# Performance work log

Measured on AMD Instinct MI355X. Metric: run time of the kernel, lower is better.

## Reference

```python
import jax, jax.numpy as jnp
import numpy as np

B, N, DIN = 16, 1024, 256
HEADS, OUT_DIM = 4, 256
F = OUT_DIM // HEADS  # per-head feature dim
NEG_SLOPE = 0.2
MASK_VAL = -1e9


def setup_inputs() -> dict:
    key = jax.random.key(0)
    k1, k2, k3, k4, k5, k6 = jax.random.split(key, 6)
    x = jax.random.normal(k1, (B, N, DIN), dtype=jnp.float32)
    adj = jax.random.uniform(k2, (B, N, N), dtype=jnp.float32)  # >0.5 -> edge
    # GATConv learned params (Glorot-ish scale)
    W = jax.random.normal(k3, (DIN, HEADS, F), dtype=jnp.float32) * (1.0 / np.sqrt(DIN))
    a_src = jax.random.normal(k4, (HEADS, F), dtype=jnp.float32) * (1.0 / np.sqrt(F))
    a_dst = jax.random.normal(k5, (HEADS, F), dtype=jnp.float32) * (1.0 / np.sqrt(F))
    bias = jax.random.normal(k6, (OUT_DIM,), dtype=jnp.float32) * 0.01
    return {"x": x, "adj": adj, "W": W, "a_src": a_src, "a_dst": a_dst, "bias": bias}


def reference(x, adj, W, a_src, a_dst, bias):
    # GAT over a dense adjacency mask: mathematically identical to
    # per-sample tf.where edge extraction + edge-list GATConv (softmax over
    # j with adj[b,i,j] > 0.5), but fully vectorized over the batch.
    b, n, _ = x.shape
    h = jnp.einsum('bnd,dhf->bnhf', x, W)                  # [B,N,H,F]
    e_src = jnp.einsum('bnhf,hf->bhn', h, a_src)           # source logits
    e_dst = jnp.einsum('bnhf,hf->bhn', h, a_dst)           # target logits
    # e[b,h,i,j]: edge j -> i
    e = e_dst[:, :, :, None] + e_src[:, :, None, :]        # [B,H,N,N]
    e = jax.nn.leaky_relu(e, NEG_SLOPE)
    mask = (adj > 0.5)[:, None, :, :]                      # [B,1,N,N]
    e = jnp.where(mask, e, MASK_VAL)
    attn = jax.nn.softmax(e, axis=-1)                      # softmax over sources j
    out = jnp.einsum('bhij,bjhf->bihf', attn, h)           # aggregate messages
    out = out.reshape(b, n, HEADS * F) + bias              # concat heads + bias
    return out
```

## Files before the change

### kernel.cpp

```cpp
#include <hip/hip_runtime.h>

#define B_    16
#define N_    1024
#define DIN_  256
#define H_    4
#define F_    64
#define COUT_ 256
#define NEG_  0.2f
#define LOG2E_ 1.4426950408889634f

typedef __bf16 bf16x8 __attribute__((ext_vector_type(8)));
typedef float  f32x4  __attribute__((ext_vector_type(4)));
typedef unsigned short u16x8 __attribute__((ext_vector_type(8)));
typedef unsigned short u16x4 __attribute__((ext_vector_type(4)));
typedef unsigned int   u32x4 __attribute__((ext_vector_type(4)));

__device__ __forceinline__ unsigned short f2bf(float f) {
    unsigned u = __builtin_bit_cast(unsigned, f);
    u += 0x7fffu + ((u >> 16) & 1u);
    return (unsigned short)(u >> 16);
}

__global__ __launch_bounds__(256) void prep_kernel(
    const float* __restrict__ W, unsigned short* __restrict__ Wtp) {
    const int c = blockIdx.x, k = threadIdx.x;
    const int w = c >> 6, ft = (c >> 4) & 3, l15 = c & 15;
    const int it = k >> 5, q = (k >> 3) & 3, jj = k & 7;
    const int ln = q * 16 + l15;
    Wtp[((((w * 8 + it) * 4 + ft) * 64) + ln) * 8 + jj] = f2bf(W[k * COUT_ + c]);
}

__global__ __launch_bounds__(256, 4) void stage_kernel(
    const float* __restrict__ adj, const float* __restrict__ x,
    const unsigned short* __restrict__ Wtp, const float* __restrict__ a_src,
    const float* __restrict__ a_dst, unsigned int* __restrict__ mask,
    unsigned short* __restrict__ hp, float* __restrict__ e_src,
    float* __restrict__ e_dst) {
    __shared__ unsigned short xs[16][264];
    const int w  = threadIdx.x >> 6;
    const int ln = threadIdx.x & 63;

    if (blockIdx.x < 4096) {
        const int row = blockIdx.x * 4 + w;
        const int b = row >> 10, i = row & (N_ - 1);
        const float* ar = adj + (size_t)row * N_ + ln * 4;
#pragma unroll
        for (int c = 0; c < 4; c++) {
            f32x4 v = *(const f32x4*)(ar + c * 256);
            unsigned nib = 0;
#pragma unroll
            for (int e = 0; e < 4; e++)
                nib |= (v[e] > 0.5f) ? (1u << e) : 0u;
            unsigned word = nib << ((ln & 7) * 4);
            word |= __shfl_xor(word, 1);
            word |= __shfl_xor(word, 2);
            word |= __shfl_xor(word, 4);
            if ((ln & 7) == 0) {
                const int jc = c * 8 + (ln >> 3);
                mask[(b * 32 + jc) * N_ + i] = word;
            }
        }
    } else {
        const int blk = blockIdx.x - 4096;
        const int b   = blk & 15;
        const int it0 = (blk >> 4) * 16;
        const int l15 = ln & 15;
        const int q   = ln >> 4;

#pragma unroll
        for (int s = 0; s < 4; s++) {
            const int row = w * 4 + s;
            f32x4 xv = *(const f32x4*)(x + (size_t)(b * N_ + it0 + row) * DIN_ + ln * 4);
            unsigned lo = (unsigned)f2bf(xv[0]) | ((unsigned)f2bf(xv[1]) << 16);
            unsigned hi = (unsigned)f2bf(xv[2]) | ((unsigned)f2bf(xv[3]) << 16);
            unsigned long long hb = (unsigned long long)lo | ((unsigned long long)hi << 32);
            *(unsigned long long*)&xs[row][ln * 4] = hb;
        }
        __syncthreads();

        f32x4 acc[4];
#pragma unroll
        for (int ft = 0; ft < 4; ft++) acc[ft] = (f32x4)0.0f;

        const unsigned short* wb = Wtp + (w * 8) * 4 * 64 * 8 + ln * 8;
#pragma unroll
        for (int it = 0; it < 8; it++) {
            bf16x8 af = *(const bf16x8*)&xs[l15][it * 32 + q * 8];
#pragma unroll
            for (int ft = 0; ft < 4; ft++) {
                bf16x8 bf = *((const bf16x8*)(wb + (it * 4 + ft) * 512));
                acc[ft] = __builtin_amdgcn_mfma_f32_16x16x32_bf16(af, bf, acc[ft], 0, 0, 0);
            }
        }

        const int jg = it0 >> 5;
        const int q2 = 2 * ((it0 >> 4) & 1) + (q >> 1);
#pragma unroll
        for (int ft = 0; ft < 4; ft++) {
            u16x4 hb;
#pragma unroll
            for (int r = 0; r < 4; r++) hb[r] = f2bf(acc[ft][r]);
            const size_t addr =
                (size_t)((((b * H_ + w) * 32 + jg) * 4 + ft) * 64 + q2 * 16 + l15) * 8 + (q & 1) * 4;
            *((u16x4*)(hp + addr)) = hb;
        }

        float as_v[4], ad_v[4];
#pragma unroll
        for (int ft = 0; ft < 4; ft++) {
            as_v[ft] = a_src[w * F_ + ft * 16 + l15];
            ad_v[ft] = a_dst[w * F_ + ft * 16 + l15];
        }
        float ps[4], pd[4];
#pragma unroll
        for (int r = 0; r < 4; r++) {
            ps[r] = 0.0f; pd[r] = 0.0f;
#pragma unroll
            for (int ft = 0; ft < 4; ft++) {
                ps[r] += acc[ft][r] * as_v[ft];
                pd[r] += acc[ft][r] * ad_v[ft];
            }
        }
#pragma unroll
        for (int off = 1; off <= 8; off <<= 1)
#pragma unroll
            for (int r = 0; r < 4; r++) {
                ps[r] += __shfl_xor(ps[r], off);
                pd[r] += __shfl_xor(pd[r], off);
            }
        float vs = (l15 == 0) ? ps[0] : (l15 == 1) ? ps[1] : (l15 == 2) ? ps[2] : ps[3];
        float vd = (l15 == 0) ? pd[0] : (l15 == 1) ? pd[1] : (l15 == 2) ? pd[2] : pd[3];
        if (l15 < 4) {
            const int i = it0 + q * 4 + l15;
            e_src[(b * H_ + w) * N_ + i] = vs * LOG2E_;
            e_dst[(b * H_ + w) * N_ + i] = vd * LOG2E_;
        }
    }
}

__global__ __launch_bounds__(512, 4) void gat_attn_kernel(
    const unsigned int* __restrict__ mask, const unsigned short* __restrict__ hp,
    const float* __restrict__ e_src, const float* __restrict__ e_dst,
    const float* __restrict__ bias, float* __restrict__ out) {
    const int lid = ((blockIdx.x & 7) << 6) | (blockIdx.x >> 3);
    const int b   = lid >> 5;
    const int it0 = (lid & 31) * 32;
    const int w8  = threadIdx.x >> 6;
    const int h   = w8 & 3;
    const int jh  = w8 >> 2;
    const int ln  = threadIdx.x & 63;
    const int l15 = ln & 15;
    const int q   = ln >> 4;

    __shared__ float lds[H_][2][5][64][4];
    __shared__ float es_s[H_][N_];
    __shared__ unsigned mk_s[32][32];

    {
        const int tid = threadIdx.x;
#pragma unroll
        for (int p = 0; p < 2; p++) {
            const int c  = p * 512 + tid;
            const int h_ = c >> 8;
            const int of = (c & 255) * 4;
            *(f32x4*)&es_s[h_][of] =
                *(const f32x4*)(e_src + (size_t)(b * H_ + h_) * N_ + of);
        }
        if (tid < 256) {
            const int jc = tid >> 3;
            const int i4 = (tid & 7) * 4;
            *(u32x4*)&mk_s[jc][i4] =
                *(const u32x4*)(mask + (size_t)(b * 32 + jc) * N_ + it0 + i4);
        }
    }

    float edv[2];
    edv[0] = e_dst[(b * H_ + h) * N_ + it0 + l15];
    edv[1] = e_dst[(b * H_ + h) * N_ + it0 + 16 + l15];

    const unsigned short* hp_base = hp + (size_t)((b * H_ + h) * 32) * 2048 + ln * 8;

    f32x4 acc[2][4];
    f32x4 accs[2];
#pragma unroll
    for (int mt = 0; mt < 2; mt++) {
#pragma unroll
        for (int ft = 0; ft < 4; ft++) acc[mt][ft] = (f32x4)0.0f;
        accs[mt] = (f32x4)0.0f;
    }

    u16x8 ones_u;
#pragma unroll
    for (int jj = 0; jj < 8; jj++) ones_u[jj] = 0x3F80;
    const bf16x8 ones = __builtin_bit_cast(bf16x8, ones_u);

    __syncthreads();

    const unsigned short* hf0 = hp_base + (size_t)(jh * 16) * 2048;
    bf16x8 nb0 = *((const bf16x8*)(hf0 + 0 * 512));
    bf16x8 nb1 = *((const bf16x8*)(hf0 + 1 * 512));
    bf16x8 nb2 = *((const bf16x8*)(hf0 + 2 * 512));
    bf16x8 nb3 = *((const bf16x8*)(hf0 + 3 * 512));

#pragma unroll
    for (int t = 0; t < 16; t++) {
        const int jg = jh * 16 + t;
        const bf16x8 cb0 = nb0, cb1 = nb1, cb2 = nb2, cb3 = nb3;
        if (t < 15) {
            const unsigned short* hfn = hp_base + (size_t)(jg + 1) * 2048;
            nb0 = *((const bf16x8*)(hfn + 0 * 512));
            nb1 = *((const bf16x8*)(hfn + 1 * 512));
            nb2 = *((const bf16x8*)(hfn + 2 * 512));
            nb3 = *((const bf16x8*)(hfn + 3 * 512));
        }

        f32x4 e0 = *(const f32x4*)&es_s[h][jg * 32 + q * 8];
        f32x4 e1 = *(const f32x4*)&es_s[h][jg * 32 + q * 8 + 4];
        const unsigned m0 = mk_s[jg][l15];
        const unsigned m1 = mk_s[jg][16 + l15];

        float es8[8] = {e0[0], e0[1], e0[2], e0[3], e1[0], e1[1], e1[2], e1[3]};

        bf16x8 afr[2];
#pragma unroll
        for (int mt = 0; mt < 2; mt++) {
            const unsigned mq = ((mt ? m1 : m0) >> (q * 8)) & 0xffu;
            u32x4 up;
#pragma unroll
            for (int p2 = 0; p2 < 4; p2++) {
                float t0 = edv[mt] + es8[2 * p2];
                float t1 = edv[mt] + es8[2 * p2 + 1];
                t0 = fmaxf(t0, NEG_ * t0);
                t1 = fmaxf(t1, NEG_ * t1);
                float p0 = __builtin_amdgcn_exp2f(t0);
                float p1 = __builtin_amdgcn_exp2f(t1);
                p0 = ((mq >> (2 * p2)) & 1u) ? p0 : 0.0f;
                p1 = ((mq >> (2 * p2 + 1)) & 1u) ? p1 : 0.0f;
                up[p2] = __builtin_amdgcn_perm(__builtin_bit_cast(unsigned, p1),
                                               __builtin_bit_cast(unsigned, p0),
                                               0x07060302u);
            }
            afr[mt] = __builtin_bit_cast(bf16x8, up);
        }
#pragma unroll
        for (int mt = 0; mt < 2; mt++) {
            acc[mt][0] = __builtin_amdgcn_mfma_f32_16x16x32_bf16(afr[mt], cb0, acc[mt][0], 0, 0, 0);
            acc[mt][1] = __builtin_amdgcn_mfma_f32_16x16x32_bf16(afr[mt], cb1, acc[mt][1], 0, 0, 0);
            acc[mt][2] = __builtin_amdgcn_mfma_f32_16x16x32_bf16(afr[mt], cb2, acc[mt][2], 0, 0, 0);
            acc[mt][3] = __builtin_amdgcn_mfma_f32_16x16x32_bf16(afr[mt], cb3, acc[mt][3], 0, 0, 0);
            accs[mt]   = __builtin_amdgcn_mfma_f32_16x16x32_bf16(afr[mt], ones, accs[mt], 0, 0, 0);
        }
    }

    if (jh == 1) {
#pragma unroll
        for (int mt = 0; mt < 2; mt++) {
#pragma unroll
            for (int ft = 0; ft < 4; ft++)
                *(f32x4*)&lds[h][mt][ft][ln][0] = acc[mt][ft];
            *(f32x4*)&lds[h][mt][4][ln][0] = accs[mt];
        }
    }
    __syncthreads();
    if (jh == 0) {
#pragma unroll
        for (int mt = 0; mt < 2; mt++) {
#pragma unroll
            for (int ft = 0; ft < 4; ft++)
                acc[mt][ft] += *(const f32x4*)&lds[h][mt][ft][ln][0];
            accs[mt] += *(const f32x4*)&lds[h][mt][4][ln][0];
        }
        float bias_v[4];
#pragma unroll
        for (int ft = 0; ft < 4; ft++) bias_v[ft] = bias[h * F_ + ft * 16 + l15];
#pragma unroll
        for (int mt = 0; mt < 2; mt++) {
            f32x4 rinv;
#pragma unroll
            for (int r = 0; r < 4; r++) rinv[r] = 1.0f / accs[mt][r];
#pragma unroll
            for (int ft = 0; ft < 4; ft++)
#pragma unroll
                for (int r = 0; r < 4; r++) {
                    const int i = it0 + mt * 16 + q * 4 + r;
                    const int c = h * F_ + ft * 16 + l15;
                    out[(size_t)(b * N_ + i) * COUT_ + c] = acc[mt][ft][r] * rinv[r] + bias_v[ft];
                }
        }
    }
}

extern "C" void kernel_launch(void* const* d_in, const int* in_sizes, int n_in,
                              void* d_out, int out_size, void* d_ws, size_t ws_size,
                              hipStream_t stream) {
    const float* x     = (const float*)d_in[0];
    const float* adj   = (const float*)d_in[1];
    const float* W     = (const float*)d_in[2];
    const float* a_src = (const float*)d_in[3];
    const float* a_dst = (const float*)d_in[4];
    const float* bias  = (const float*)d_in[5];
    float* out = (float*)d_out;

    char* ws = (char*)d_ws;
    unsigned short* Wtp = (unsigned short*)ws;
    unsigned short* hp  = (unsigned short*)(ws + 131072);
    float* e_src        = (float*)(ws + 131072 + 8388608);
    float* e_dst        = (float*)(ws + 131072 + 8388608 + 262144);
    unsigned int* mask  = (unsigned int*)(ws + 131072 + 8388608 + 524288);

    prep_kernel<<<256, 256, 0, stream>>>(W, Wtp);
    stage_kernel<<<5120, 256, 0, stream>>>(adj, x, Wtp, a_src, a_dst, mask, hp, e_src, e_dst);
    gat_attn_kernel<<<512, 512, 0, stream>>>(mask, hp, e_src, e_dst, bias, out);
}
```

Before: 149.0 us.

## Build adjacency bitmask with wave ballots and store row-major permuted bit layout

Mask construction now uses per-lane ballots in place of nibble packing plus three xor shuffles, and each row's 32 mask words are written contiguously instead of as strided scattered stores. The attention kernel loads the row-major mask into padded shared memory (transposed indexing) and decodes bits with a permuted bit mapping that matches the ballot layout. The goal is cheaper mask generation and coalesced mask writes. The cost is 16 ballots per wave and scalar shared stores on the attention side.

```diff
diff --git a/kernel.cpp b/kernel.cpp
--- a/kernel.cpp
+++ b/kernel.cpp
@@ -42,24 +42,34 @@
 
     if (blockIdx.x < 4096) {
         const int row = blockIdx.x * 4 + w;
-        const int b = row >> 10, i = row & (N_ - 1);
         const float* ar = adj + (size_t)row * N_ + ln * 4;
-#pragma unroll
-        for (int c = 0; c < 4; c++) {
-            f32x4 v = *(const f32x4*)(ar + c * 256);
-            unsigned nib = 0;
-#pragma unroll
-            for (int e = 0; e < 4; e++)
-                nib |= (v[e] > 0.5f) ? (1u << e) : 0u;
-            unsigned word = nib << ((ln & 7) * 4);
-            word |= __shfl_xor(word, 1);
-            word |= __shfl_xor(word, 2);
-            word |= __shfl_xor(word, 4);
-            if ((ln & 7) == 0) {
-                const int jc = c * 8 + (ln >> 3);
-                mask[(b * 32 + jc) * N_ + i] = word;
-            }
-        }
+
+        f32x4 v0 = *(const f32x4*)(ar);
+        f32x4 v1 = *(const f32x4*)(ar + 256);
+        f32x4 v2 = *(const f32x4*)(ar + 512);
+        f32x4 v3 = *(const f32x4*)(ar + 768);
+
+        unsigned long long bal[4][4];
+#pragma unroll
+        for (int e = 0; e < 4; e++) {
+            bal[0][e] = __ballot(v0[e] > 0.5f);
+            bal[1][e] = __ballot(v1[e] > 0.5f);
+            bal[2][e] = __ballot(v2[e] > 0.5f);
+            bal[3][e] = __ballot(v3[e] > 0.5f);
+        }
+
+        const int c_ = (ln >> 3) & 3;
+        const int sh = (ln & 7) * 8;
+        unsigned wd = 0;
+#pragma unroll
+        for (int e = 0; e < 4; e++) {
+            unsigned long long be = (c_ == 0) ? bal[0][e]
+                                  : (c_ == 1) ? bal[1][e]
+                                  : (c_ == 2) ? bal[2][e] : bal[3][e];
+            wd |= ((unsigned)((be >> sh) & 0xffull)) << (8 * e);
+        }
+        if (ln < 32)
+            mask[(size_t)row * 32 + ln] = wd;
     } else {
         const int blk = blockIdx.x - 4096;
         const int b   = blk & 15;
@@ -154,7 +164,7 @@
 
     __shared__ float lds[H_][2][5][64][4];
     __shared__ float es_s[H_][N_];
-    __shared__ unsigned mk_s[32][32];
+    __shared__ unsigned mk_s[32][37];
 
     {
         const int tid = threadIdx.x;
@@ -167,10 +177,13 @@
                 *(const f32x4*)(e_src + (size_t)(b * H_ + h_) * N_ + of);
         }
         if (tid < 256) {
-            const int jc = tid >> 3;
-            const int i4 = (tid & 7) * 4;
-            *(u32x4*)&mk_s[jc][i4] =
-                *(const u32x4*)(mask + (size_t)(b * 32 + jc) * N_ + it0 + i4);
+            const int ii  = tid >> 3;
+            const int jc4 = (tid & 7) * 4;
+            u32x4 mv = *(const u32x4*)(mask + ((size_t)(b * N_ + it0 + ii)) * 32 + jc4);
+            mk_s[ii][jc4 + 0] = mv[0];
+            mk_s[ii][jc4 + 1] = mv[1];
+            mk_s[ii][jc4 + 2] = mv[2];
+            mk_s[ii][jc4 + 3] = mv[3];
         }
     }
 
@@ -201,6 +214,9 @@
     bf16x8 nb1 = *((const bf16x8*)(hf0 + 1 * 512));
     bf16x8 nb2 = *((const bf16x8*)(hf0 + 2 * 512));
     bf16x8 nb3 = *((const bf16x8*)(hf0 + 3 * 512));
+
+    const int bp0[4] = {0, 16, 1, 17};
+    const int bp1[4] = {8, 24, 9, 25};
 
 #pragma unroll
     for (int t = 0; t < 16; t++) {
@@ -216,15 +232,15 @@
 
         f32x4 e0 = *(const f32x4*)&es_s[h][jg * 32 + q * 8];
         f32x4 e1 = *(const f32x4*)&es_s[h][jg * 32 + q * 8 + 4];
-        const unsigned m0 = mk_s[jg][l15];
-        const unsigned m1 = mk_s[jg][16 + l15];
+        const unsigned w0 = mk_s[l15][jg] >> (2 * q);
+        const unsigned w1 = mk_s[16 + l15][jg] >> (2 * q);
 
         float es8[8] = {e0[0], e0[1], e0[2], e0[3], e1[0], e1[1], e1[2], e1[3]};
 
         bf16x8 afr[2];
 #pragma unroll
         for (int mt = 0; mt < 2; mt++) {
-            const unsigned mq = ((mt ? m1 : m0) >> (q * 8)) & 0xffu;
+            const unsigned mw = mt ? w1 : w0;
             u32x4 up;
 #pragma unroll
             for (int p2 = 0; p2 < 4; p2++) {
@@ -234,8 +250,8 @@
                 t1 = fmaxf(t1, NEG_ * t1);
                 float p0 = __builtin_amdgcn_exp2f(t0);
                 float p1 = __builtin_amdgcn_exp2f(t1);
-                p0 = ((mq >> (2 * p2)) & 1u) ? p0 : 0.0f;
-                p1 = ((mq >> (2 * p2 + 1)) & 1u) ? p1 : 0.0f;
+                p0 = ((mw >> bp0[p2]) & 1u) ? p0 : 0.0f;
+                p1 = ((mw >> bp1[p2]) & 1u) ? p1 : 0.0f;
                 up[p2] = __builtin_amdgcn_perm(__builtin_bit_cast(unsigned, p1),
                                                __builtin_bit_cast(unsigned, p0),
                                                0x07060302u);
```

Measured after the change: 142.5 us. 4.4% less time.
